# Optimization experiments

Hardware: AMD Instinct MI355X
Metric: run time of the kernel (lower is better)

## Reference

```python
import jax, jax.numpy as jnp
import numpy as np

N_NODES = 100000
N_EDGES = 1600000
F_IN = 128
HID = 64
N_CLASSES = 1
N_GRAPHS = 1024


def gcn_conv(x, src, dst, deg_inv_sqrt, W, b):
    # PyG GCNConv: out = D^{-1/2}(A+I)D^{-1/2} X W + b
    xw = x @ W  # [N, H]
    norm = deg_inv_sqrt[src] * deg_inv_sqrt[dst]  # [E]
    msg = xw[src] * norm[:, None]  # gather + scale
    agg = jax.ops.segment_sum(msg, dst, num_segments=N_NODES)
    # self-loop contribution: norm_ii = deg_inv_sqrt[i]^2
    agg = agg + xw * (deg_inv_sqrt ** 2)[:, None]
    return agg + b


def setup_inputs() -> dict:
    key = jax.random.key(0)
    ks = jax.random.split(key, 12)
    x = jax.random.normal(ks[0], (N_NODES, F_IN), dtype=jnp.float32)
    edge_index = jax.random.randint(ks[1], (2, N_EDGES), 0, N_NODES, dtype=jnp.int64)
    batch = jnp.sort(jax.random.randint(ks[2], (N_NODES,), 0, N_GRAPHS, dtype=jnp.int64))
    def glorot(k, fan_in, fan_out):
        s = (6.0 / (fan_in + fan_out)) ** 0.5
        return jax.random.uniform(k, (fan_in, fan_out), dtype=jnp.float32, minval=-s, maxval=s)
    W1 = glorot(ks[3], F_IN, HID); b1 = jnp.zeros((HID,), jnp.float32)
    W2 = glorot(ks[4], HID, HID); b2 = jnp.zeros((HID,), jnp.float32)
    W3 = glorot(ks[5], HID, HID); b3 = jnp.zeros((HID,), jnp.float32)
    Wl = glorot(ks[6], HID, N_CLASSES); bl = jnp.zeros((N_CLASSES,), jnp.float32)
    return {"x": x, "edge_index": edge_index, "batch": batch,
            "W1": W1, "b1": b1, "W2": W2, "b2": b2, "W3": W3, "b3": b3,
            "Wl": Wl, "bl": bl}


def reference(x, edge_index, batch, W1, b1, W2, b2, W3, b3, Wl, bl):
    src, dst = edge_index[0], edge_index[1]
    # degree with self-loops: deg[i] = (# incoming edges at i) + 1
    deg = jax.ops.segment_sum(jnp.ones((N_EDGES,), x.dtype), dst, num_segments=N_NODES) + 1.0
    deg_inv_sqrt = jax.lax.rsqrt(deg)
    h = jax.nn.relu(gcn_conv(x, src, dst, deg_inv_sqrt, W1, b1))
    # dropout: identity in eval mode
    h = jax.nn.relu(gcn_conv(h, src, dst, deg_inv_sqrt, W2, b2))
    h = gcn_conv(h, src, dst, deg_inv_sqrt, W3, b3)
    # global_mean_pool over graph ids
    sums = jax.ops.segment_sum(h, batch, num_segments=N_GRAPHS)
    counts = jax.ops.segment_sum(jnp.ones((N_NODES,), h.dtype), batch, num_segments=N_GRAPHS)
    pooled = sums / jnp.maximum(counts, 1.0)[:, None]  # [G, HID]
    return pooled @ Wl + bl  # [G, num_classes]
```

## Files before the change

kernel.cpp:

```cpp
#include <hip/hip_runtime.h>
#include <hip/hip_bf16.h>

#define N_NODES 100000
#define N_EDGES 1600000
#define F_IN 128
#define HID 64
#define N_GRAPHS 1024

#define SH 9
#define NBU 196
#define NB 200
#define BCAP 9728
#define EPB 8192
#define NSLICE 4

typedef __attribute__((ext_vector_type(8))) short bf16x8;
typedef __attribute__((ext_vector_type(4))) float f32x4;
typedef __attribute__((ext_vector_type(4))) unsigned int u32x4;

__device__ __forceinline__ unsigned short f2bf(float f) {
    __hip_bfloat16 h = __float2bfloat16(f);
    return *reinterpret_cast<unsigned short*>(&h);
}
__device__ __forceinline__ float bf2f(unsigned int u) {
    return __uint_as_float(u << 16);
}

__device__ __forceinline__ float loadf(const void* p, size_t i, int f32) {
    if (f32) return ((const float*)p)[i];
    return __bfloat162float(((const __hip_bfloat16*)p)[i]);
}
__device__ __forceinline__ int loadi(const void* p, size_t i, int i64) {
    if (i64) return (int)((const long long*)p)[i];
    return ((const int*)p)[i];
}

__global__ void k_init(const unsigned int* __restrict__ xw_,
                       const unsigned int* __restrict__ ei_,
                       int* __restrict__ flags,
                       int* __restrict__ gcnt, int* __restrict__ bcnt) {
    __shared__ int cnt_f, cnt_i;
    int t = threadIdx.x;
    if (t == 0) { cnt_f = 0; cnt_i = 0; }
    __syncthreads();
    unsigned int w = xw_[t];
    unsigned int e = (w >> 7) & 0xFFu;
    if (e >= 100u && e <= 140u) atomicAdd(&cnt_f, 1);
    unsigned int iw = ei_[2 * t + 1];
    if (iw == 0u) atomicAdd(&cnt_i, 1);
    for (int i = t; i < N_GRAPHS; i += 256) gcnt[i] = 0;
    for (int i = t; i < NB; i += 256) bcnt[i] = 0;
    __syncthreads();
    if (t == 0) {
        flags[0] = (cnt_f < 180) ? 1 : 0;
        flags[1] = (cnt_i >= 128) ? 1 : 0;
    }
}

__global__ __launch_bounds__(256) void k_part(const void* __restrict__ ei,
                                              const void* __restrict__ batch,
                                              int* __restrict__ bcnt,
                                              int* __restrict__ gcnt,
                                              unsigned int* __restrict__ packed,
                                              const int* __restrict__ flags) {
    int I64 = flags[1];
    __shared__ int hist[NB];
    __shared__ int base[NB];
    __shared__ int ghist[N_GRAPHS];
    int t = threadIdx.x;
    if (t < NB) hist[t] = 0;
    for (int i = t; i < N_GRAPHS; i += 256) ghist[i] = 0;
    __syncthreads();
    for (int it = 0; it < 2; ++it) {
        int n = blockIdx.x * 512 + it * 256 + t;
        if (n < N_NODES) atomicAdd(&ghist[loadi(batch, n, I64)], 1);
    }
    int e0 = blockIdx.x * EPB;
#pragma unroll 4
    for (int it = 0; it < EPB / 256; ++it) {
        int e = e0 + it * 256 + t;
        if (e < N_EDGES) {
            int d = loadi(ei, (size_t)N_EDGES + e, I64);
            atomicAdd(&hist[d >> SH], 1);
        }
    }
    __syncthreads();
    if (t < NB) {
        base[t] = hist[t] ? atomicAdd(&bcnt[t], hist[t]) : 0;
        hist[t] = 0;
    }
    for (int i = t; i < N_GRAPHS; i += 256)
        if (ghist[i]) atomicAdd(&gcnt[i], ghist[i]);
    __syncthreads();
#pragma unroll 4
    for (int it = 0; it < EPB / 256; ++it) {
        int e = e0 + it * 256 + t;
        if (e < N_EDGES) {
            int s = loadi(ei, e, I64);
            int d = loadi(ei, (size_t)N_EDGES + e, I64);
            int b = d >> SH;
            int r = atomicAdd(&hist[b], 1);
            int pos = base[b] + r;
            if (pos < BCAP)
                packed[(size_t)b * BCAP + pos] = ((unsigned int)s << SH) | (unsigned int)(d & 511);
        }
    }
}

__global__ __launch_bounds__(256) void k_hist(const unsigned int* __restrict__ packed,
                                              const int* __restrict__ bcnt,
                                              int* __restrict__ cnt,
                                              float* __restrict__ dis,
                                              int* __restrict__ partN) {
    __shared__ int hist[512];
    int b = blockIdx.x;
    int t = threadIdx.x;
    int n = bcnt[b];
    if (n > BCAP) n = BCAP;
    for (int i = t; i < 512; i += 256) hist[i] = 0;
    __syncthreads();
    const unsigned int* pb = packed + (size_t)b * BCAP;
    for (int i = t; i < n; i += 256)
        atomicAdd(&hist[pb[i] & 511u], 1);
    __syncthreads();
    int nbase = b << SH;
    for (int i = t; i < 512; i += 256) {
        int node = nbase + i;
        if (node < N_NODES) {
            int c = hist[i];
            cnt[node] = c;
            dis[node] = rsqrtf((float)c + 1.0f);
        }
    }
    __syncthreads();
    for (int off = 128; off > 0; off >>= 1) {
        if (t < off) { hist[t] += hist[t + off]; hist[256 + t] += hist[256 + t + off]; }
        __syncthreads();
    }
    if (t == 0) {
        partN[2 * b] = hist[0];
        if (2 * b + 1 < 391) partN[2 * b + 1] = hist[256];
    }
}

__global__ void k_scan_mid(int* __restrict__ partial, int nb,
                           int* __restrict__ rp, int n,
                           const int* __restrict__ gcnt, int* __restrict__ gptr) {
    __shared__ int s[512];
    int t = threadIdx.x;
    int v = (t < nb) ? partial[t] : 0;
    s[t] = v;
    __syncthreads();
    for (int off = 1; off < 512; off <<= 1) {
        int x = (t >= off) ? s[t - off] : 0;
        __syncthreads();
        s[t] += x;
        __syncthreads();
    }
    if (t < nb) partial[t] = s[t] - v;
    if (t == 511) rp[n] = s[511];
    __syncthreads();
    int a = gcnt[2 * t], bq = gcnt[2 * t + 1];
    int ps = a + bq;
    s[t] = ps;
    __syncthreads();
    for (int off = 1; off < 512; off <<= 1) {
        int x = (t >= off) ? s[t - off] : 0;
        __syncthreads();
        s[t] += x;
        __syncthreads();
    }
    int excl = s[t] - ps;
    gptr[2 * t] = excl;
    gptr[2 * t + 1] = excl + a;
    if (t == 511) gptr[1024] = s[511];
}

__global__ void k_scan_p3(const int* __restrict__ in, const int* __restrict__ partial,
                          int* __restrict__ out, int n) {
    __shared__ int s[256];
    int t = threadIdx.x;
    int i = blockIdx.x * 256 + t;
    int v = (i < n) ? in[i] : 0;
    s[t] = v;
    __syncthreads();
    for (int off = 1; off < 256; off <<= 1) {
        int x = (t >= off) ? s[t - off] : 0;
        __syncthreads();
        s[t] += x;
        __syncthreads();
    }
    if (i < n) out[i] = partial[blockIdx.x] + s[t] - v;
}

__global__ __launch_bounds__(512) void k_bucketcsr(const unsigned int* __restrict__ packed,
                                                   const int* __restrict__ bcnt,
                                                   const int* __restrict__ rp,
                                                   int* __restrict__ csr) {
    __shared__ int offs[512];
    __shared__ int elds[BCAP];
    int b = blockIdx.x;
    int nbase = b << SH;
    int base = rp[nbase];
    int lim = nbase + 512; if (lim > N_NODES) lim = N_NODES;
    int nedge = rp[lim] - base;
    if (nedge > BCAP) nedge = BCAP;
    for (int i = threadIdx.x; i < 512; i += 512) {
        int node = nbase + i;
        offs[i] = (node < N_NODES) ? (rp[node] - base) : nedge;
    }
    __syncthreads();
    int n = bcnt[b]; if (n > BCAP) n = BCAP;
    const unsigned int* pb = packed + (size_t)b * BCAP;
    for (int i = threadIdx.x; i < n; i += 512) {
        unsigned int p = pb[i];
        int pos = atomicAdd(&offs[p & 511u], 1);
        if (pos < BCAP) elds[pos] = (int)(p >> SH);
    }
    __syncthreads();
    for (int i = threadIdx.x; i < nedge; i += 512)
        csr[base + i] = elds[i];
}

template <int K>
__global__ __launch_bounds__(256) void k_gemm(const void* __restrict__ x,
                                              const void* __restrict__ W,
                                              const float* __restrict__ dis,
                                              unsigned short* __restrict__ out,
                                              const int* __restrict__ flags,
                                              int x_is_f32, int in_sm) {
    int Wf32 = flags[0];
    int xF32 = (x_is_f32 < 0) ? Wf32 : x_is_f32;
    __shared__ unsigned short Wt[64][K + 8];
    __shared__ unsigned short xs[32][K + 8];
    int t = threadIdx.x;
    int wave = t >> 6, lane = t & 63;
    int quad = lane >> 4, l16 = lane & 15;

    for (int id = t; id < 64 * K; id += 256) {
        int k = id >> 6, n = id & 63;
        Wt[n][k] = f2bf(loadf(W, id, Wf32));
    }
    __syncthreads();

    bf16x8 bfrag[K / 32];
#pragma unroll
    for (int c = 0; c < K / 32; ++c)
        bfrag[c] = *reinterpret_cast<bf16x8*>(&Wt[wave * 16 + l16][c * 32 + quad * 8]);

    const int ngroups = (N_NODES + 31) / 32;
    for (int g = blockIdx.x; g < ngroups; g += gridDim.x) {
        __syncthreads();
        int row0 = g * 32;
        if (in_sm) {
            for (int cid = t; cid < 4 * K; cid += 256) {
                int slice = cid >> 6, i = cid & 63;
                int rr = i >> 1, half = i & 1;
                int r = row0 + rr;
                u32x4 val = {0u, 0u, 0u, 0u};
                if (r < N_NODES)
                    val = ((const u32x4*)x)[((size_t)slice * N_NODES + row0) * 2 + i];
                *reinterpret_cast<u32x4*>(&xs[rr][slice * 16 + half * 8]) = val;
            }
        } else {
            for (int cid = t; cid < 4 * K; cid += 256) {
                int rr = cid / (K / 8), c8 = cid % (K / 8);
                int r = row0 + rr;
                u32x4 val = {0u, 0u, 0u, 0u};
                if (r < N_NODES) {
                    size_t base = (size_t)r * K + c8 * 8;
                    if (xF32) {
                        const u32x4* xp = (const u32x4*)x;
                        u32x4 q0 = xp[base / 4];
                        u32x4 q1 = xp[base / 4 + 1];
                        val.x = f2bf(__uint_as_float(q0.x)) | ((unsigned int)f2bf(__uint_as_float(q0.y)) << 16);
                        val.y = f2bf(__uint_as_float(q0.z)) | ((unsigned int)f2bf(__uint_as_float(q0.w)) << 16);
                        val.z = f2bf(__uint_as_float(q1.x)) | ((unsigned int)f2bf(__uint_as_float(q1.y)) << 16);
                        val.w = f2bf(__uint_as_float(q1.z)) | ((unsigned int)f2bf(__uint_as_float(q1.w)) << 16);
                    } else {
                        val = ((const u32x4*)x)[base / 8];
                    }
                }
                *reinterpret_cast<u32x4*>(&xs[rr][c8 * 8]) = val;
            }
        }
        __syncthreads();

        f32x4 acc0 = {0.f, 0.f, 0.f, 0.f};
        f32x4 acc1 = {0.f, 0.f, 0.f, 0.f};
#pragma unroll
        for (int c = 0; c < K / 32; ++c) {
            bf16x8 a0 = *reinterpret_cast<bf16x8*>(&xs[l16][c * 32 + quad * 8]);
            bf16x8 a1 = *reinterpret_cast<bf16x8*>(&xs[16 + l16][c * 32 + quad * 8]);
            acc0 = __builtin_amdgcn_mfma_f32_16x16x32_bf16(a0, bfrag[c], acc0, 0, 0, 0);
            acc1 = __builtin_amdgcn_mfma_f32_16x16x32_bf16(a1, bfrag[c], acc1, 0, 0, 0);
        }
        unsigned short* ow = out + (size_t)wave * (N_NODES * 16);
#pragma unroll
        for (int reg = 0; reg < 4; ++reg) {
            int r0 = row0 + quad * 4 + reg;
            if (r0 < N_NODES) ow[(size_t)r0 * 16 + l16] = f2bf(acc0[reg] * dis[r0]);
            int r1 = row0 + 16 + quad * 4 + reg;
            if (r1 < N_NODES) ow[(size_t)r1 * 16 + l16] = f2bf(acc1[reg] * dis[r1]);
        }
    }
}

__global__ __launch_bounds__(256) void k_gather_sm(const int* __restrict__ rp,
                                                   const int* __restrict__ csr,
                                                   const float* __restrict__ dis,
                                                   const unsigned short* __restrict__ xws,
                                                   const void* __restrict__ bias,
                                                   unsigned short* __restrict__ out,
                                                   int do_relu,
                                                   const int* __restrict__ flags) {
    int F32 = flags[0];
    int blk = blockIdx.x;
    int xcd = blk & 7;
    int s = xcd >> 1;
    int grp = ((blk >> 3) << 1) | (xcd & 1);
    int wave = threadIdx.x >> 6, lane = threadIdx.x & 63;
    int nodesub = lane >> 4;
    int eslot = (lane >> 1) & 7;
    int half = lane & 1;
    const u32x4* xs4 = (const u32x4*)(xws + (size_t)s * N_NODES * 16);
    u32x4* op = (u32x4*)out + (size_t)s * N_NODES * 2;
    float bb0 = loadf(bias, s * 16 + half * 8 + 0, F32);
    float bb1 = loadf(bias, s * 16 + half * 8 + 1, F32);
    float bb2 = loadf(bias, s * 16 + half * 8 + 2, F32);
    float bb3 = loadf(bias, s * 16 + half * 8 + 3, F32);
    float bb4 = loadf(bias, s * 16 + half * 8 + 4, F32);
    float bb5 = loadf(bias, s * 16 + half * 8 + 5, F32);
    float bb6 = loadf(bias, s * 16 + half * 8 + 6, F32);
    float bb7 = loadf(bias, s * 16 + half * 8 + 7, F32);
    int wbase = grp * 64 + wave * 16;

    for (int ni = 0; ni < 4; ++ni) {
        int node = wbase + ni * 4 + nodesub;
        int valid = node < N_NODES;
        int start = valid ? rp[node] : 0;
        int end = valid ? rp[node + 1] : 0;
        float a0 = 0.f, a1 = 0.f, a2 = 0.f, a3 = 0.f;
        float a4 = 0.f, a5 = 0.f, a6 = 0.f, a7 = 0.f;
        int j = start + eslot;
        if (j < end) {
            int src = csr[j];
            for (;;) {
                int jn = j + 8;
                int sn = (jn < end) ? csr[jn] : 0;
                u32x4 v = xs4[(size_t)src * 2 + half];
                a0 += bf2f(v.x & 0xFFFFu); a1 += bf2f(v.x >> 16);
                a2 += bf2f(v.y & 0xFFFFu); a3 += bf2f(v.y >> 16);
                a4 += bf2f(v.z & 0xFFFFu); a5 += bf2f(v.z >> 16);
                a6 += bf2f(v.w & 0xFFFFu); a7 += bf2f(v.w >> 16);
                if (jn >= end) break;
                j = jn; src = sn;
            }
        }
#pragma unroll
        for (int off = 2; off <= 8; off <<= 1) {
            a0 += __shfl_down(a0, off, 64); a1 += __shfl_down(a1, off, 64);
            a2 += __shfl_down(a2, off, 64); a3 += __shfl_down(a3, off, 64);
            a4 += __shfl_down(a4, off, 64); a5 += __shfl_down(a5, off, 64);
            a6 += __shfl_down(a6, off, 64); a7 += __shfl_down(a7, off, 64);
        }
        if (((lane & 14) == 0) && valid) {
            u32x4 sv = xs4[(size_t)node * 2 + half];
            float dn = dis[node];
            float v0 = fmaf(a0 + bf2f(sv.x & 0xFFFFu), dn, bb0);
            float v1 = fmaf(a1 + bf2f(sv.x >> 16),     dn, bb1);
            float v2 = fmaf(a2 + bf2f(sv.y & 0xFFFFu), dn, bb2);
            float v3 = fmaf(a3 + bf2f(sv.y >> 16),     dn, bb3);
            float v4 = fmaf(a4 + bf2f(sv.z & 0xFFFFu), dn, bb4);
            float v5 = fmaf(a5 + bf2f(sv.z >> 16),     dn, bb5);
            float v6 = fmaf(a6 + bf2f(sv.w & 0xFFFFu), dn, bb6);
            float v7 = fmaf(a7 + bf2f(sv.w >> 16),     dn, bb7);
            if (do_relu) {
                v0 = fmaxf(v0, 0.f); v1 = fmaxf(v1, 0.f); v2 = fmaxf(v2, 0.f); v3 = fmaxf(v3, 0.f);
                v4 = fmaxf(v4, 0.f); v5 = fmaxf(v5, 0.f); v6 = fmaxf(v6, 0.f); v7 = fmaxf(v7, 0.f);
            }
            u32x4 o;
            o.x = (unsigned int)f2bf(v0) | ((unsigned int)f2bf(v1) << 16);
            o.y = (unsigned int)f2bf(v2) | ((unsigned int)f2bf(v3) << 16);
            o.z = (unsigned int)f2bf(v4) | ((unsigned int)f2bf(v5) << 16);
            o.w = (unsigned int)f2bf(v6) | ((unsigned int)f2bf(v7) << 16);
            op[(size_t)node * 2 + half] = o;
        }
    }
}

__global__ __launch_bounds__(256) void k_pool_final(const int* __restrict__ gptr,
                             const unsigned short* __restrict__ h,
                             const void* __restrict__ Wl, const void* __restrict__ bl,
                             void* __restrict__ out, const int* __restrict__ flags) {
    int F32 = flags[0];
    int g = blockIdx.x * 4 + (threadIdx.x >> 6);
    int lane = threadIdx.x & 63;
    if (g >= N_GRAPHS) return;
    int s = gptr[g], e = gptr[g + 1];
    size_t hbase = (size_t)(lane >> 4) * N_NODES * 16 + (lane & 15);
    float acc = 0.0f;
    for (int n = s; n < e; ++n) acc += bf2f(h[hbase + (size_t)n * 16]);
    float cnt = fmaxf((float)(e - s), 1.0f);
    float v = (acc / cnt) * loadf(Wl, lane, F32);
#pragma unroll
    for (int o = 32; o > 0; o >>= 1) v += __shfl_down(v, o, 64);
    if (lane == 0) {
        float r = v + loadf(bl, 0, F32);
        if (F32) ((float*)out)[g] = r;
        else     ((__hip_bfloat16*)out)[g] = __float2bfloat16(r);
    }
}

extern "C" void kernel_launch(void* const* d_in, const int* in_sizes, int n_in,
                              void* d_out, int out_size, void* d_ws, size_t ws_size,
                              hipStream_t stream) {
    const void* x     = d_in[0];
    const void* ei    = d_in[1];
    const void* batch = d_in[2];
    const void* W1 = d_in[3];
    const void* b1 = d_in[4];
    const void* W2 = d_in[5];
    const void* b2 = d_in[6];
    const void* W3 = d_in[7];
    const void* b3 = d_in[8];
    const void* Wl = d_in[9];
    const void* bl = d_in[10];

    float* dis   = (float*)d_ws;
    int*   cnt   = (int*)(dis + 100352);
    int*   rp    = cnt + 100352;
    int*   csr   = rp + 100352;
    int*   gcnt  = csr + 1600000;
    int*   gptr  = gcnt + 1024;
    int*   partN = gptr + 1056;
    int*   bcnt  = partN + 512;
    int*   flags = bcnt + 256;
    unsigned int* packed = (unsigned int*)(flags + 16);
    unsigned short* bufA = (unsigned short*)(packed + (size_t)NB * BCAP);
    unsigned short* bufB = bufA + (size_t)NSLICE * N_NODES * 16;

    const int TB = 256;
    dim3 blk(TB);
    int gN = (N_NODES + TB - 1) / TB;
    int gGA = 782 * 8;

    k_init<<<1, blk, 0, stream>>>((const unsigned int*)x, (const unsigned int*)ei,
                                  flags, gcnt, bcnt);
    k_part<<<(N_EDGES + EPB - 1) / EPB, blk, 0, stream>>>(ei, batch, bcnt, gcnt, packed, flags);
    k_hist<<<NBU, blk, 0, stream>>>(packed, bcnt, cnt, dis, partN);
    k_scan_mid<<<1, 512, 0, stream>>>(partN, gN, rp, N_NODES, gcnt, gptr);
    k_scan_p3<<<gN, blk, 0, stream>>>(cnt, partN, rp, N_NODES);
    k_bucketcsr<<<NBU, 512, 0, stream>>>(packed, bcnt, rp, csr);

    k_gemm<F_IN><<<1024, blk, 0, stream>>>(x, W1, dis, bufA, flags, -1, 0);
    k_gather_sm<<<gGA, blk, 0, stream>>>(rp, csr, dis, bufA, b1, bufB, 1, flags);
    k_gemm<HID><<<1024, blk, 0, stream>>>(bufB, W2, dis, bufA, flags, 0, 1);
    k_gather_sm<<<gGA, blk, 0, stream>>>(rp, csr, dis, bufA, b2, bufB, 1, flags);
    k_gemm<HID><<<1024, blk, 0, stream>>>(bufB, W3, dis, bufA, flags, 0, 1);
    k_gather_sm<<<gGA, blk, 0, stream>>>(rp, csr, dis, bufA, b3, bufB, 0, flags);

    k_pool_final<<<N_GRAPHS / 4, blk, 0, stream>>>(gptr, bufB, Wl, bl, d_out, flags);
}
```

Measured before the change: 378.7 us.

## Stage edges in LDS, dual-issue gather loads, widen pooling per graph

```diff
diff --git a/kernel.cpp b/kernel.cpp
--- a/kernel.cpp
+++ b/kernel.cpp
@@ -67,6 +67,8 @@
     __shared__ int hist[NB];
     __shared__ int base[NB];
     __shared__ int ghist[N_GRAPHS];
+    __shared__ unsigned int elds[EPB];
+    __shared__ unsigned char ebkt[EPB];
     int t = threadIdx.x;
     if (t < NB) hist[t] = 0;
     for (int i = t; i < N_GRAPHS; i += 256) ghist[i] = 0;
@@ -78,11 +80,19 @@
     int e0 = blockIdx.x * EPB;
 #pragma unroll 4
     for (int it = 0; it < EPB / 256; ++it) {
-        int e = e0 + it * 256 + t;
+        int idx = it * 256 + t;
+        int e = e0 + idx;
+        unsigned int pv = 0u;
+        unsigned char bk = 0xFFu;
         if (e < N_EDGES) {
+            int sN = loadi(ei, e, I64);
             int d = loadi(ei, (size_t)N_EDGES + e, I64);
+            bk = (unsigned char)(d >> SH);
+            pv = ((unsigned int)sN << SH) | (unsigned int)(d & 511);
             atomicAdd(&hist[d >> SH], 1);
         }
+        elds[idx] = pv;
+        ebkt[idx] = bk;
     }
     __syncthreads();
     if (t < NB) {
@@ -94,15 +104,14 @@
     __syncthreads();
 #pragma unroll 4
     for (int it = 0; it < EPB / 256; ++it) {
-        int e = e0 + it * 256 + t;
-        if (e < N_EDGES) {
-            int s = loadi(ei, e, I64);
-            int d = loadi(ei, (size_t)N_EDGES + e, I64);
-            int b = d >> SH;
-            int r = atomicAdd(&hist[b], 1);
-            int pos = base[b] + r;
+        int idx = it * 256 + t;
+        unsigned char bk = ebkt[idx];
+        if (bk != 0xFFu) {
+            unsigned int pv = elds[idx];
+            int r = atomicAdd(&hist[bk], 1);
+            int pos = base[bk] + r;
             if (pos < BCAP)
-                packed[(size_t)b * BCAP + pos] = ((unsigned int)s << SH) | (unsigned int)(d & 511);
+                packed[(size_t)bk * BCAP + pos] = pv;
         }
     }
 }
@@ -342,19 +351,31 @@
         int end = valid ? rp[node + 1] : 0;
         float a0 = 0.f, a1 = 0.f, a2 = 0.f, a3 = 0.f;
         float a4 = 0.f, a5 = 0.f, a6 = 0.f, a7 = 0.f;
-        int j = start + eslot;
-        if (j < end) {
-            int src = csr[j];
+        int ja = start + eslot;
+        if (ja < end) {
+            int jb = ja + 8;
+            int sa = csr[ja];
+            int okb = (jb < end);
+            int sb = okb ? csr[jb] : sa;
             for (;;) {
-                int jn = j + 8;
-                int sn = (jn < end) ? csr[jn] : 0;
-                u32x4 v = xs4[(size_t)src * 2 + half];
-                a0 += bf2f(v.x & 0xFFFFu); a1 += bf2f(v.x >> 16);
-                a2 += bf2f(v.y & 0xFFFFu); a3 += bf2f(v.y >> 16);
-                a4 += bf2f(v.z & 0xFFFFu); a5 += bf2f(v.z >> 16);
-                a6 += bf2f(v.w & 0xFFFFu); a7 += bf2f(v.w >> 16);
-                if (jn >= end) break;
-                j = jn; src = sn;
+                u32x4 va = xs4[(size_t)sa * 2 + half];
+                u32x4 vb = xs4[(size_t)sb * 2 + half];
+                int jan = ja + 16, jbn = jb + 16;
+                int san = (jan < end) ? csr[jan] : 0;
+                int sbn = (jbn < end) ? csr[jbn] : 0;
+                a0 += bf2f(va.x & 0xFFFFu); a1 += bf2f(va.x >> 16);
+                a2 += bf2f(va.y & 0xFFFFu); a3 += bf2f(va.y >> 16);
+                a4 += bf2f(va.z & 0xFFFFu); a5 += bf2f(va.z >> 16);
+                a6 += bf2f(va.w & 0xFFFFu); a7 += bf2f(va.w >> 16);
+                if (okb) {
+                    a0 += bf2f(vb.x & 0xFFFFu); a1 += bf2f(vb.x >> 16);
+                    a2 += bf2f(vb.y & 0xFFFFu); a3 += bf2f(vb.y >> 16);
+                    a4 += bf2f(vb.z & 0xFFFFu); a5 += bf2f(vb.z >> 16);
+                    a6 += bf2f(vb.w & 0xFFFFu); a7 += bf2f(vb.w >> 16);
+                }
+                if (jan >= end) break;
+                ja = jan; jb = jbn; sa = san; sb = sbn;
+                okb = (jbn < end);
             }
         }
 #pragma unroll
@@ -394,19 +415,35 @@
                              const void* __restrict__ Wl, const void* __restrict__ bl,
                              void* __restrict__ out, const int* __restrict__ flags) {
     int F32 = flags[0];
-    int g = blockIdx.x * 4 + (threadIdx.x >> 6);
+    __shared__ float part[4];
+    int g = blockIdx.x;
+    int s = threadIdx.x >> 6;
     int lane = threadIdx.x & 63;
-    if (g >= N_GRAPHS) return;
-    int s = gptr[g], e = gptr[g + 1];
-    size_t hbase = (size_t)(lane >> 4) * N_NODES * 16 + (lane & 15);
-    float acc = 0.0f;
-    for (int n = s; n < e; ++n) acc += bf2f(h[hbase + (size_t)n * 16]);
-    float cnt = fmaxf((float)(e - s), 1.0f);
-    float v = (acc / cnt) * loadf(Wl, lane, F32);
-#pragma unroll
-    for (int o = 32; o > 0; o >>= 1) v += __shfl_down(v, o, 64);
-    if (lane == 0) {
-        float r = v + loadf(bl, 0, F32);
+    int nsub = lane >> 3, up = lane & 7;
+    int s0 = gptr[g], e0 = gptr[g + 1];
+    const unsigned int* xsl = (const unsigned int*)h + (size_t)s * N_NODES * 8;
+    float a0 = 0.f, a1 = 0.f;
+    for (int n = s0 + nsub; n < e0; n += 8) {
+        unsigned int v = xsl[(size_t)n * 8 + up];
+        a0 += bf2f(v & 0xFFFFu);
+        a1 += bf2f(v >> 16);
+    }
+    a0 += __shfl_down(a0, 32, 64); a1 += __shfl_down(a1, 32, 64);
+    a0 += __shfl_down(a0, 16, 64); a1 += __shfl_down(a1, 16, 64);
+    a0 += __shfl_down(a0, 8, 64);  a1 += __shfl_down(a1, 8, 64);
+    float v = 0.f;
+    if (nsub == 0) {
+        float cnt = fmaxf((float)(e0 - s0), 1.0f);
+        int f = s * 16 + up * 2;
+        v = (a0 / cnt) * loadf(Wl, f, F32) + (a1 / cnt) * loadf(Wl, f + 1, F32);
+    }
+    v += __shfl_down(v, 4, 64);
+    v += __shfl_down(v, 2, 64);
+    v += __shfl_down(v, 1, 64);
+    if (lane == 0) part[s] = v;
+    __syncthreads();
+    if (threadIdx.x == 0) {
+        float r = part[0] + part[1] + part[2] + part[3] + loadf(bl, 0, F32);
         if (F32) ((float*)out)[g] = r;
         else     ((__hip_bfloat16*)out)[g] = __float2bfloat16(r);
     }
@@ -460,5 +497,5 @@
     k_gemm<HID><<<1024, blk, 0, stream>>>(bufB, W3, dis, bufA, flags, 0, 1);
     k_gather_sm<<<gGA, blk, 0, stream>>>(rp, csr, dis, bufA, b3, bufB, 0, flags);
 
-    k_pool_final<<<N_GRAPHS / 4, blk, 0, stream>>>(gptr, bufB, Wl, bl, d_out, flags);
-}
+    k_pool_final<<<N_GRAPHS, blk, 0, stream>>>(gptr, bufB, Wl, bl, d_out, flags);
+}
```

After: 361.7 us. -4.5%, faster.
